# Performance work log

Hardware: AMD Instinct MI355X
Metric: run time of the kernel (lower is better)

The kernel has to match this reference:

```python
import jax, jax.numpy as jnp
import numpy as np

TURBO_BLOCK_SIZE = 64
TURBO_MSE_BITS = 5
QMAX = 2 ** (TURBO_MSE_BITS - 1) - 1  # 15 for symmetric int5
# MSE scale search grid: shrink factors applied to the max-abs scale
SHRINKS = np.linspace(0.4, 1.0, 16)


def mse_quant_dequant(w):
    """Block-wise (block=64, along input dim) symmetric int5 quantize-dequantize.
    Per block, searches a grid of shrunken max-abs scales and keeps the one
    minimizing reconstruction MSE."""
    O, I = w.shape
    wb = w.reshape(O, I // TURBO_BLOCK_SIZE, TURBO_BLOCK_SIZE)
    amax = jnp.max(jnp.abs(wb), axis=-1, keepdims=True)
    base = jnp.maximum(amax, 1e-8) / QMAX
    best_err = jnp.full(amax.shape, jnp.inf, dtype=w.dtype)
    best_scale = base
    for s in SHRINKS:  # fixed small grid, not a data-dim loop
        scale = base * jnp.asarray(s, dtype=w.dtype)
        deq = jnp.clip(jnp.round(wb / scale), -QMAX, QMAX) * scale
        err = jnp.sum((deq - wb) ** 2, axis=-1, keepdims=True)
        upd = err < best_err
        best_err = jnp.where(upd, err, best_err)
        best_scale = jnp.where(upd, scale, best_scale)
    deq = jnp.clip(jnp.round(wb / best_scale), -QMAX, QMAX) * best_scale
    return deq.reshape(O, I)


def turbo_linear(x, w):
    # Straight-through estimator: forward uses quantized weights,
    # gradient flows to w as identity.
    wq = w + jax.lax.stop_gradient(mse_quant_dequant(w) - w)
    return x @ wq.T


def setup_inputs() -> dict:
    key = jax.random.key(0)
    k1, k2, k3 = jax.random.split(key, 3)
    dim, mlp_mult = 2048, 4
    hidden = mlp_mult * dim
    x = jax.random.normal(k1, (4, 2048, dim), dtype=jnp.float32)
    w_fc = jax.random.normal(k2, (hidden, dim), dtype=jnp.float32) * 0.02
    w_proj = jax.random.normal(k3, (dim, hidden), dtype=jnp.float32) * 0.02
    return {"x": x, "w_fc": w_fc, "w_proj": w_proj}


def reference(x, w_fc, w_proj):
    h = jnp.maximum(turbo_linear(x, w_fc), 0.0)  # relu
    return turbo_linear(h * h, w_proj)           # relu-square then proj
```

## Files before the change

kernel.cpp:

```cpp
#include <hip/hip_runtime.h>
#include <hip/hip_bf16.h>

typedef __attribute__((ext_vector_type(8))) __bf16 bf16x8;
typedef __attribute__((ext_vector_type(4))) float f32x4;

__device__ __forceinline__ void gload_lds16(const void* g, void* lds) {
    __builtin_amdgcn_global_load_lds(
        (const __attribute__((address_space(1))) void*)g,
        (__attribute__((address_space(3))) void*)lds, 16, 0, 0);
}

__global__ __launch_bounds__(256) void quant_bf16_kernel(
    const float* __restrict__ w, __hip_bfloat16* __restrict__ wq, int nblk)
{
#pragma clang fp contract(off)
    int b = blockIdx.x * 256 + threadIdx.x;
    if (b >= nblk) return;
    const float4* src = (const float4*)(w + (size_t)b * 64);
    float v[64];
#pragma unroll
    for (int i = 0; i < 16; ++i) {
        float4 t = src[i];
        v[i*4+0] = t.x; v[i*4+1] = t.y; v[i*4+2] = t.z; v[i*4+3] = t.w;
    }
    float amax = 0.0f;
#pragma unroll
    for (int i = 0; i < 64; ++i) amax = fmaxf(amax, fabsf(v[i]));
    float base = fmaxf(amax, 1e-8f) / 15.0f;

    float best_err = __builtin_inff();
    float best_scale = base, best_rs = 0.0f;
    for (int k = 0; k < 16; ++k) {
        double sd = (k == 15) ? 1.0 : ((double)k * (0.6 / 15.0) + 0.4);
        float scale = base * (float)sd;
        float rs = 1.0f / scale;
        float err = 0.0f;
#pragma unroll
        for (int i = 0; i < 64; ++i) {
            float q = rintf(v[i] * rs);
            q = fminf(fmaxf(q, -15.0f), 15.0f);
            float d = q * scale - v[i];
            err = err + d * d;
        }
        if (err < best_err) { best_err = err; best_scale = scale; best_rs = rs; }
    }
    __hip_bfloat16* dst = wq + (size_t)b * 64;
#pragma unroll
    for (int i = 0; i < 64; ++i) {
        float q = rintf(v[i] * best_rs);
        q = fminf(fmaxf(q, -15.0f), 15.0f);
        dst[i] = __float2bfloat16(q * best_scale);
    }
}

__global__ __launch_bounds__(256) void f32_to_bf16_kernel(
    const float* __restrict__ in, __hip_bfloat16* __restrict__ out, int n8)
{
    int i = blockIdx.x * 256 + threadIdx.x;
    if (i >= n8) return;
    const float4* p = (const float4*)(in + (size_t)i * 8);
    float4 a = p[0], b = p[1];
    alignas(16) __hip_bfloat16 r[8];
    r[0] = __float2bfloat16(a.x); r[1] = __float2bfloat16(a.y);
    r[2] = __float2bfloat16(a.z); r[3] = __float2bfloat16(a.w);
    r[4] = __float2bfloat16(b.x); r[5] = __float2bfloat16(b.y);
    r[6] = __float2bfloat16(b.z); r[7] = __float2bfloat16(b.w);
    *(uint4*)(out + (size_t)i * 8) = *(const uint4*)r;
}

template <int EPI>
__global__ __launch_bounds__(512, 1) void gemm256_kernel(
    const __hip_bfloat16* __restrict__ A,
    const __hip_bfloat16* __restrict__ B,
    void* __restrict__ Cout, int M, int N, int K)
{
    extern __shared__ char smem[];

    const int t    = threadIdx.x;
    const int lane = t & 63;
    const int w    = t >> 6;
    const int wr   = w >> 2;
    const int wc   = w & 3;
    const int lo   = lane & 15;
    const int hi   = lane >> 4;

    const int cpx = gridDim.x >> 3;
    int bid = blockIdx.x;
    bid = (bid & 7) * cpx + (bid >> 3);
    const int nN = N >> 8;
    const int bm = bid / nN;
    const int bn = bid % nN;
    const int rowBase = bm << 8;
    const int colBase = bn << 8;

    uint offA[2], offB[2];
#pragma unroll
    for (int r = 0; r < 2; ++r) {
        uint o = (uint)r * 8192u + (uint)t * 16u;
        uint p = o ^ (((o >> 7) & 7u) << 4);
        uint srow = p >> 7;
        uint scol = (p & 127u) >> 1;
        offA[r] = (uint)(rowBase + srow) * (uint)K + scol;
        offB[r] = (uint)(colBase + srow) * (uint)K + scol;
    }
    const uint hG = 128u * (uint)K;

    const uint sw   = (uint)(lo & 7) << 4;
    const uint aB   = (uint)wr * 16384u + (uint)lo * 128u;
    const uint bB   = 32768u + (uint)(wc >> 1) * 16384u
                    + ((uint)(wc & 1) * 64u + (uint)lo) * 128u;
    const uint cb0  = ((uint)hi * 16u) ^ sw;
    const uint cb1  = (64u + (uint)hi * 16u) ^ sw;

    f32x4 acc[8][4] = {};
    bf16x8 bfrag[4][2];

    {
        char* d = smem + (uint)w * 1024u;
#pragma unroll
        for (int r = 0; r < 2; ++r) {
            char* dr = d + r * 8192;
            gload_lds16(A + offA[r],      dr + 0);
            gload_lds16(A + offA[r] + hG, dr + 16384);
            gload_lds16(B + offB[r],      dr + 32768);
            gload_lds16(B + offB[r] + hG, dr + 49152);
        }
    }
    asm volatile("s_waitcnt vmcnt(0)" ::: "memory");
    __builtin_amdgcn_s_barrier();

    const int NT = K >> 6;
    uint k0 = 64;
    for (int tile = 0; tile < NT; ++tile) {
        const uint bufOff = (uint)(tile & 1) * 65536u;
        char* nb = smem + (uint)((tile + 1) & 1) * 65536u;
        const bool pf = (tile + 1 < NT);
#pragma unroll
        for (int ph = 0; ph < 4; ++ph) {
            bf16x8 afrag[2][2];
#pragma unroll
            for (int di = 0; di < 2; ++di) {
                const uint ab = bufOff + aB + (uint)(2*ph + di) * 2048u;
                afrag[di][0] = *(const bf16x8*)(smem + ab + cb0);
                afrag[di][1] = *(const bf16x8*)(smem + ab + cb1);
            }
            if (ph == 0) {
#pragma unroll
                for (int j = 0; j < 4; ++j) {
                    const uint bb = bufOff + bB + (uint)j * 2048u;
                    bfrag[j][0] = *(const bf16x8*)(smem + bb + cb0);
                    bfrag[j][1] = *(const bf16x8*)(smem + bb + cb1);
                }
                if (pf) {
                    char* d = nb + (uint)w * 1024u;
                    gload_lds16(A + (size_t)(offA[0] + k0),      d + 0);
                    gload_lds16(A + (size_t)(offA[1] + k0),      d + 8192);
                    gload_lds16(A + (size_t)(offA[0] + hG + k0), d + 16384);
                    gload_lds16(A + (size_t)(offA[1] + hG + k0), d + 16384 + 8192);
                    gload_lds16(B + (size_t)(offB[0] + k0),      d + 32768);
                    gload_lds16(B + (size_t)(offB[1] + k0),      d + 32768 + 8192);
                    gload_lds16(B + (size_t)(offB[0] + hG + k0), d + 49152);
                    gload_lds16(B + (size_t)(offB[1] + hG + k0), d + 49152 + 8192);
                }
            }
            __builtin_amdgcn_s_barrier();
            asm volatile("s_waitcnt lgkmcnt(0)" ::: "memory");
            __builtin_amdgcn_s_setprio(1);
#pragma unroll
            for (int di = 0; di < 2; ++di)
#pragma unroll
                for (int j = 0; j < 4; ++j) {
                    acc[2*ph+di][j] = __builtin_amdgcn_mfma_f32_16x16x32_bf16(
                        afrag[di][0], bfrag[j][0], acc[2*ph+di][j], 0, 0, 0);
                    acc[2*ph+di][j] = __builtin_amdgcn_mfma_f32_16x16x32_bf16(
                        afrag[di][1], bfrag[j][1], acc[2*ph+di][j], 0, 0, 0);
                }
            __builtin_amdgcn_s_setprio(0);
            if (ph == 3) asm volatile("s_waitcnt vmcnt(0)" ::: "memory");
            __builtin_amdgcn_s_barrier();
        }
        k0 += 64;
    }

    if (EPI == 0) {
        __hip_bfloat16* Cb = (__hip_bfloat16*)Cout;
#pragma unroll
        for (int i = 0; i < 8; ++i)
#pragma unroll
            for (int j = 0; j < 4; ++j)
#pragma unroll
                for (int r = 0; r < 4; ++r) {
                    size_t row = rowBase + wr*128 + i*16 + hi*4 + r;
                    size_t col = colBase + wc*64 + j*16 + lo;
                    float v = fmaxf(acc[i][j][r], 0.0f);
                    Cb[row * N + col] = __float2bfloat16(v * v);
                }
    } else {
        float* Cf = (float*)Cout;
#pragma unroll
        for (int i = 0; i < 8; ++i)
#pragma unroll
            for (int j = 0; j < 4; ++j)
#pragma unroll
                for (int r = 0; r < 4; ++r) {
                    size_t row = rowBase + wr*128 + i*16 + hi*4 + r;
                    size_t col = colBase + wc*64 + j*16 + lo;
                    Cf[row * N + col] = acc[i][j][r];
                }
    }
}

extern "C" void kernel_launch(void* const* d_in, const int* in_sizes, int n_in,
                              void* d_out, int out_size, void* d_ws, size_t ws_size,
                              hipStream_t stream) {
    const float* x      = (const float*)d_in[0];
    const float* w_fc   = (const float*)d_in[1];
    const float* w_proj = (const float*)d_in[2];
    float* out = (float*)d_out;

    const int DIM = 2048, HID = 8192, M = 8192;

    char* ws = (char*)d_ws;
    __hip_bfloat16* Xb  = (__hip_bfloat16*)ws;
    __hip_bfloat16* Wfc = (__hip_bfloat16*)(ws + (size_t)M * DIM * 2);
    __hip_bfloat16* Wpj = (__hip_bfloat16*)(ws + (size_t)(M * DIM + (size_t)HID * DIM) * 2);
    __hip_bfloat16* H2  = (__hip_bfloat16*)(ws + (size_t)(M * DIM + 2 * (size_t)HID * DIM) * 2);

    (void)hipFuncSetAttribute((const void*)gemm256_kernel<0>,
                              hipFuncAttributeMaxDynamicSharedMemorySize, 131072);
    (void)hipFuncSetAttribute((const void*)gemm256_kernel<1>,
                              hipFuncAttributeMaxDynamicSharedMemorySize, 131072);

    int nblk = HID * DIM / 64;
    quant_bf16_kernel<<<nblk / 256, 256, 0, stream>>>(w_fc, Wfc, nblk);
    quant_bf16_kernel<<<nblk / 256, 256, 0, stream>>>(w_proj, Wpj, nblk);

    int n8 = M * DIM / 8;
    f32_to_bf16_kernel<<<n8 / 256, 256, 0, stream>>>(x, Xb, n8);

    gemm256_kernel<0><<<(M/256)*(HID/256), 512, 131072, stream>>>(
        Xb, Wfc, (void*)H2, M, HID, DIM);

    gemm256_kernel<1><<<(M/256)*(DIM/256), 512, 131072, stream>>>(
        H2, Wpj, (void*)out, M, DIM, HID);
}
```

Baseline: 632.6 us.

## Stagger GEMM global-to-LDS prefetch across phases with partial vmcnt waits

Restructures the GEMM main loop to process two K-tiles per iteration and spreads the global-to-LDS loads for upcoming tiles over all eight MFMA phases instead of issuing them all at phase 0. B tiles are fetched further ahead into the opposite buffer, and waits use vmcnt(4) so some loads stay in flight across barriers. The goal is to smooth memory traffic and hide load latency behind MFMA work. In exchange, buffer reuse timing becomes more intricate, and the loop assumes K is a multiple of 128.

New measurement: 611.3 us. 3.4% less time.

```diff
diff --git a/kernel.cpp b/kernel.cpp
--- a/kernel.cpp
+++ b/kernel.cpp
@@ -83,6 +83,7 @@
     const int wc   = w & 3;
     const int lo   = lane & 15;
     const int hi   = lane >> 4;
+    const uint wOff = (uint)w * 1024u;
 
     const int cpx = gridDim.x >> 3;
     int bid = blockIdx.x;
@@ -93,76 +94,97 @@
     const int rowBase = bm << 8;
     const int colBase = bn << 8;
 
-    uint offA[2], offB[2];
-#pragma unroll
-    for (int r = 0; r < 2; ++r) {
-        uint o = (uint)r * 8192u + (uint)t * 16u;
-        uint p = o ^ (((o >> 7) & 7u) << 4);
-        uint srow = p >> 7;
-        uint scol = (p & 127u) >> 1;
-        offA[r] = (uint)(rowBase + srow) * (uint)K + scol;
-        offB[r] = (uint)(colBase + srow) * (uint)K + scol;
+    uint offA0, offA1, offB0, offB1;
+    {
+        uint o0 = (uint)t * 16u;
+        uint o1 = 8192u + (uint)t * 16u;
+        uint p0 = o0 ^ (((o0 >> 7) & 7u) << 4);
+        uint p1 = o1 ^ (((o1 >> 7) & 7u) << 4);
+        uint r0 = p0 >> 7, c0 = (p0 & 127u) >> 1;
+        uint r1 = p1 >> 7, c1 = (p1 & 127u) >> 1;
+        offA0 = (uint)(rowBase + r0) * (uint)K + c0;
+        offA1 = (uint)(rowBase + r1) * (uint)K + c1;
+        offB0 = (uint)(colBase + r0) * (uint)K + c0;
+        offB1 = (uint)(colBase + r1) * (uint)K + c1;
     }
     const uint hG = 128u * (uint)K;
 
-    const uint sw   = (uint)(lo & 7) << 4;
-    const uint aB   = (uint)wr * 16384u + (uint)lo * 128u;
-    const uint bB   = 32768u + (uint)(wc >> 1) * 16384u
-                    + ((uint)(wc & 1) * 64u + (uint)lo) * 128u;
-    const uint cb0  = ((uint)hi * 16u) ^ sw;
-    const uint cb1  = (64u + (uint)hi * 16u) ^ sw;
+    const uint sw  = (uint)(lo & 7) << 4;
+    const uint aB  = (uint)wr * 16384u + (uint)lo * 128u;
+    const uint bB  = 32768u + (uint)(wc >> 1) * 16384u
+                   + ((uint)(wc & 1) * 64u + (uint)lo) * 128u;
+    const uint cb0 = ((uint)hi * 16u) ^ sw;
+    const uint cb1 = (64u + (uint)hi * 16u) ^ sw;
 
     f32x4 acc[8][4] = {};
     bf16x8 bfrag[4][2];
 
-    {
-        char* d = smem + (uint)w * 1024u;
-#pragma unroll
-        for (int r = 0; r < 2; ++r) {
-            char* dr = d + r * 8192;
-            gload_lds16(A + offA[r],      dr + 0);
-            gload_lds16(A + offA[r] + hG, dr + 16384);
-            gload_lds16(B + offB[r],      dr + 32768);
-            gload_lds16(B + offB[r] + hG, dr + 49152);
-        }
-    }
-    asm volatile("s_waitcnt vmcnt(0)" ::: "memory");
+    gload_lds16(A + (size_t)offA0,        smem + 0     + wOff);
+    gload_lds16(A + (size_t)offA1,        smem + 8192  + wOff);
+    gload_lds16(A + (size_t)(offA0 + hG), smem + 16384 + wOff);
+    gload_lds16(A + (size_t)(offA1 + hG), smem + 24576 + wOff);
+    gload_lds16(B + (size_t)offB0,        smem + 32768 + wOff);
+    gload_lds16(B + (size_t)offB1,        smem + 40960 + wOff);
+    gload_lds16(B + (size_t)(offB0 + hG), smem + 49152 + wOff);
+    gload_lds16(B + (size_t)(offB1 + hG), smem + 57344 + wOff);
+    gload_lds16(B + (size_t)(offB0 + 64),      smem + 65536 + 32768 + wOff);
+    gload_lds16(B + (size_t)(offB1 + 64),      smem + 65536 + 40960 + wOff);
+    gload_lds16(B + (size_t)(offB0 + hG + 64), smem + 65536 + 49152 + wOff);
+    gload_lds16(B + (size_t)(offB1 + hG + 64), smem + 65536 + 57344 + wOff);
+    asm volatile("s_waitcnt vmcnt(4)" ::: "memory");
     __builtin_amdgcn_s_barrier();
 
-    const int NT = K >> 6;
-    uint k0 = 64;
-    for (int tile = 0; tile < NT; ++tile) {
-        const uint bufOff = (uint)(tile & 1) * 65536u;
-        char* nb = smem + (uint)((tile + 1) & 1) * 65536u;
-        const bool pf = (tile + 1 < NT);
-#pragma unroll
-        for (int ph = 0; ph < 4; ++ph) {
+    const int NI = K >> 7;
+    for (int P = 0; P < NI; ++P) {
+        const bool pf = (P + 1 < NI);
+        const uint kN1 = ((uint)(2 * P + 1)) << 6;
+        const uint kN2 = kN1 + 64;
+        const uint kN3 = kN1 + 128;
+#pragma unroll
+        for (int ph = 0; ph < 8; ++ph) {
+            const int q = ph & 3;
+            const uint bufOff = (uint)(ph >> 2) * 65536u;
             bf16x8 afrag[2][2];
 #pragma unroll
             for (int di = 0; di < 2; ++di) {
-                const uint ab = bufOff + aB + (uint)(2*ph + di) * 2048u;
+                const uint ab = bufOff + aB + (uint)(2 * q + di) * 2048u;
                 afrag[di][0] = *(const bf16x8*)(smem + ab + cb0);
                 afrag[di][1] = *(const bf16x8*)(smem + ab + cb1);
             }
-            if (ph == 0) {
+            if (q == 0) {
 #pragma unroll
                 for (int j = 0; j < 4; ++j) {
                     const uint bb = bufOff + bB + (uint)j * 2048u;
                     bfrag[j][0] = *(const bf16x8*)(smem + bb + cb0);
                     bfrag[j][1] = *(const bf16x8*)(smem + bb + cb1);
                 }
-                if (pf) {
-                    char* d = nb + (uint)w * 1024u;
-                    gload_lds16(A + (size_t)(offA[0] + k0),      d + 0);
-                    gload_lds16(A + (size_t)(offA[1] + k0),      d + 8192);
-                    gload_lds16(A + (size_t)(offA[0] + hG + k0), d + 16384);
-                    gload_lds16(A + (size_t)(offA[1] + hG + k0), d + 16384 + 8192);
-                    gload_lds16(B + (size_t)(offB[0] + k0),      d + 32768);
-                    gload_lds16(B + (size_t)(offB[1] + k0),      d + 32768 + 8192);
-                    gload_lds16(B + (size_t)(offB[0] + hG + k0), d + 49152);
-                    gload_lds16(B + (size_t)(offB[1] + hG + k0), d + 49152 + 8192);
-                }
-            }
+            }
+            if (ph == 0) {
+                gload_lds16(A + (size_t)(offA0 + kN1), smem + 65536 + 0    + wOff);
+                gload_lds16(A + (size_t)(offA1 + kN1), smem + 65536 + 8192 + wOff);
+            } else if (ph == 1) {
+                gload_lds16(A + (size_t)(offA0 + hG + kN1), smem + 65536 + 16384 + wOff);
+                gload_lds16(A + (size_t)(offA1 + hG + kN1), smem + 65536 + 24576 + wOff);
+            } else if (ph == 2) { if (pf) {
+                gload_lds16(B + (size_t)(offB0 + kN2), smem + 32768 + wOff);
+                gload_lds16(B + (size_t)(offB1 + kN2), smem + 40960 + wOff); }
+            } else if (ph == 3) { if (pf) {
+                gload_lds16(B + (size_t)(offB0 + hG + kN2), smem + 49152 + wOff);
+                gload_lds16(B + (size_t)(offB1 + hG + kN2), smem + 57344 + wOff); }
+            } else if (ph == 4) { if (pf) {
+                gload_lds16(A + (size_t)(offA0 + kN2), smem + 0    + wOff);
+                gload_lds16(A + (size_t)(offA1 + kN2), smem + 8192 + wOff); }
+            } else if (ph == 5) { if (pf) {
+                gload_lds16(A + (size_t)(offA0 + hG + kN2), smem + 16384 + wOff);
+                gload_lds16(A + (size_t)(offA1 + hG + kN2), smem + 24576 + wOff); }
+            } else if (ph == 6) { if (pf) {
+                gload_lds16(B + (size_t)(offB0 + kN3), smem + 65536 + 32768 + wOff);
+                gload_lds16(B + (size_t)(offB1 + kN3), smem + 65536 + 40960 + wOff); }
+            } else { if (pf) {
+                gload_lds16(B + (size_t)(offB0 + hG + kN3), smem + 65536 + 49152 + wOff);
+                gload_lds16(B + (size_t)(offB1 + hG + kN3), smem + 65536 + 57344 + wOff); }
+            }
+
             __builtin_amdgcn_s_barrier();
             asm volatile("s_waitcnt lgkmcnt(0)" ::: "memory");
             __builtin_amdgcn_s_setprio(1);
@@ -170,16 +192,20 @@
             for (int di = 0; di < 2; ++di)
 #pragma unroll
                 for (int j = 0; j < 4; ++j) {
-                    acc[2*ph+di][j] = __builtin_amdgcn_mfma_f32_16x16x32_bf16(
-                        afrag[di][0], bfrag[j][0], acc[2*ph+di][j], 0, 0, 0);
-                    acc[2*ph+di][j] = __builtin_amdgcn_mfma_f32_16x16x32_bf16(
-                        afrag[di][1], bfrag[j][1], acc[2*ph+di][j], 0, 0, 0);
+                    acc[2*q+di][j] = __builtin_amdgcn_mfma_f32_16x16x32_bf16(
+                        afrag[di][0], bfrag[j][0], acc[2*q+di][j], 0, 0, 0);
+                    acc[2*q+di][j] = __builtin_amdgcn_mfma_f32_16x16x32_bf16(
+                        afrag[di][1], bfrag[j][1], acc[2*q+di][j], 0, 0, 0);
                 }
             __builtin_amdgcn_s_setprio(0);
-            if (ph == 3) asm volatile("s_waitcnt vmcnt(0)" ::: "memory");
+            if (ph == 3) {
+                if (pf) asm volatile("s_waitcnt vmcnt(4)" ::: "memory");
+                else    asm volatile("s_waitcnt vmcnt(0)" ::: "memory");
+            } else if (ph == 7) {
+                if (pf) asm volatile("s_waitcnt vmcnt(4)" ::: "memory");
+            }
             __builtin_amdgcn_s_barrier();
         }
-        k0 += 64;
     }
 
     if (EPI == 0) {
```
